# Kernel tuning notes

Hardware: AMD Instinct MI355X
Metric: run time of the kernel (lower is better)

The kernel has to match this reference:

```python
import jax, jax.numpy as jnp
import numpy as np

N = 100000   # num nodes (in_channels)
D = 128      # out_channels
H = 2 * D    # hidden dim
E = 1600000  # num edges


def gcn_conv(x, W, b, src, dst, dinv):
    """PyG GCNConv: linear -> symmetric-normalized aggregation (with self loops) -> +bias."""
    xw = x @ W                                   # [N, out]
    norm = dinv[src] * dinv[dst]                 # [E]
    msg = xw[src] * norm[:, None]                # [E, out]  gather + scale
    agg = jax.ops.segment_sum(msg, dst, num_segments=N)  # scatter-add to targets
    agg = agg + xw * (dinv * dinv)[:, None]      # self-loop contribution
    return agg + b


def setup_inputs() -> dict:
    key = jax.random.key(0)
    k1, k2, k3, k4, k5, k6 = jax.random.split(key, 6)
    emb = jax.random.normal(k1, (N, D), dtype=jnp.float32)
    # Glorot-ish scaled weights
    W1 = jax.random.normal(k2, (D, H), dtype=jnp.float32) * (1.0 / np.sqrt(D))
    b1 = jnp.zeros((H,), dtype=jnp.float32)
    W2 = jax.random.normal(k3, (H, D), dtype=jnp.float32) * (1.0 / np.sqrt(H))
    b2 = jnp.zeros((D,), dtype=jnp.float32)
    edge_index = jax.random.randint(k4, (2, E), 0, N, dtype=jnp.int32).astype(jnp.int64)
    return {"emb": emb, "W1": W1, "b1": b1, "W2": W2, "b2": b2, "edge_index": edge_index}


def reference(emb, W1, b1, W2, b2, edge_index):
    src = edge_index[0]
    dst = edge_index[1]
    # degrees include the self loop added by GCNConv (add_self_loops=True)
    deg = jax.ops.segment_sum(jnp.ones((E,), dtype=emb.dtype), dst, num_segments=N) + 1.0
    dinv = jax.lax.rsqrt(deg)                    # deg >= 1, always finite
    x = gcn_conv(emb, W1, b1, src, dst, dinv)    # [N, 2D]
    x = jax.nn.relu(x)
    out = gcn_conv(x, W2, b2, src, dst, dinv)    # [N, D]
    return out
```

## Files before the change

### kernel.cpp

```cpp
#include <hip/hip_runtime.h>
#include <hip/hip_bf16.h>

#define NN 100000
#define DD 128
#define HH 256

#define NBKT 391
#define ABLK 128

typedef _Float16 half_t;
typedef _Float16 half8 __attribute__((ext_vector_type(8)));
typedef _Float16 half4_t __attribute__((ext_vector_type(4)));
typedef float floatx4 __attribute__((ext_vector_type(4)));


__global__ __launch_bounds__(256) void hist_bkt(const int* __restrict__ dst,
                                                int* __restrict__ cnt,
                                                int* __restrict__ tot,
                                                int E, int epb) {
    __shared__ int h[NBKT];
    for (int i = threadIdx.x; i < NBKT; i += 256) h[i] = 0;
    __syncthreads();
    int base = blockIdx.x * epb;
    int end = min(base + epb, E);
    for (int e = base + (int)threadIdx.x; e < end; e += 256)
        atomicAdd(&h[dst[e] >> 8], 1);
    __syncthreads();
    for (int i = threadIdx.x; i < NBKT; i += 256) {
        int v = h[i];
        cnt[i * ABLK + blockIdx.x] = v;
        if (v) atomicAdd(&tot[i], v);
    }
}

__global__ __launch_bounds__(512) void scan_all(const int* __restrict__ tot,
                                                const int* __restrict__ cnt,
                                                int* __restrict__ bktStart,
                                                int* __restrict__ blockOff) {
    __shared__ int s[512];
    int b = blockIdx.x, t = threadIdx.x;
    int v = (t < NBKT) ? tot[t] : 0;
    s[t] = v;
    __syncthreads();
    for (int off = 1; off < 512; off <<= 1) {
        int u = (t >= off) ? s[t - off] : 0;
        __syncthreads();
        s[t] += u;
        __syncthreads();
    }
    int bs = (b > 0) ? s[b - 1] : 0;
    int tail = s[NBKT - 1];
    __syncthreads();
    if (t == 0) {
        bktStart[b] = bs;
        if (b == NBKT - 1) bktStart[NBKT] = tail;
    }
    int c = (t < ABLK) ? cnt[b * ABLK + t] : 0;
    s[t] = c;
    __syncthreads();
    for (int off = 1; off < 512; off <<= 1) {
        int u = (t >= off) ? s[t - off] : 0;
        __syncthreads();
        s[t] += u;
        __syncthreads();
    }
    if (t < ABLK) blockOff[b * ABLK + t] = bs + s[t] - c;
}

__global__ __launch_bounds__(256) void part_edges(const int* __restrict__ src,
                                                  const int* __restrict__ dst,
                                                  const int* __restrict__ blockOff,
                                                  int* __restrict__ epk4,
                                                  int E, int epb) {
    __shared__ int lbase[NBKT];
    for (int i = threadIdx.x; i < NBKT; i += 256)
        lbase[i] = blockOff[i * ABLK + blockIdx.x];
    __syncthreads();
    int base = blockIdx.x * epb;
    int end = min(base + epb, E);
    for (int e = base + (int)threadIdx.x; e < end; e += 256) {
        int d = dst[e];
        int p = atomicAdd(&lbase[d >> 8], 1);
        epk4[p] = src[e] | ((d & 255) << 17);
    }
}

__global__ __launch_bounds__(256) void build_csr(const int* __restrict__ epk4,
                                                 const int* __restrict__ bktStart,
                                                 int* __restrict__ offsets,
                                                 float* __restrict__ dinv,
                                                 int* __restrict__ eidx, int N) {
    __shared__ int ncnt[256];
    __shared__ int noff[256];
    __shared__ int cur[256];
    int b = blockIdx.x, t = threadIdx.x;
    int n0 = b << 8;
    int estart = bktStart[b], eend = bktStart[b + 1];
    ncnt[t] = 0;
    __syncthreads();
    for (int e = estart + t; e < eend; e += 256)
        atomicAdd(&ncnt[epk4[e] >> 17], 1);
    __syncthreads();
    int c = ncnt[t];
    noff[t] = c;
    __syncthreads();
    for (int off = 1; off < 256; off <<= 1) {
        int u = (t >= off) ? noff[t - off] : 0;
        __syncthreads();
        noff[t] += u;
        __syncthreads();
    }
    int myoff = estart + noff[t] - c;
    cur[t] = myoff;
    int node = n0 + t;
    if (node < N) {
        offsets[node] = myoff;
        dinv[node] = rsqrtf((float)c + 1.0f);
        if (node == N - 1) offsets[N] = eend;
    }
    __syncthreads();
    for (int e = estart + t; e < eend; e += 256) {
        int p = epk4[e];
        int pos = atomicAdd(&cur[p >> 17], 1);
        eidx[pos] = p & 0x1FFFF;
    }
}

__global__ __launch_bounds__(256) void f2h_scale(const float* __restrict__ in,
                                                 const float* __restrict__ dinv,
                                                 half_t* __restrict__ out, int n4) {
    int i = blockIdx.x * 256 + threadIdx.x;
    if (i < n4) {
        float s = dinv[i >> 5];
        float4 v = ((const float4*)in)[i];
        half4_t o = {(half_t)(v.x * s), (half_t)(v.y * s), (half_t)(v.z * s), (half_t)(v.w * s)};
        ((half4_t*)out)[i] = o;
    }
}

__global__ __launch_bounds__(256) void transpose_both(const float* __restrict__ W1,
                                                      const float* __restrict__ W2,
                                                      half_t* __restrict__ W1t,
                                                      half_t* __restrict__ W2t) {
    int i = blockIdx.x * 256 + threadIdx.x;
    if (i < DD * HH) {
        int k = i / HH, c = i - k * HH;
        W1t[(size_t)c * DD + k] = (half_t)W1[i];
    } else if (i < 2 * DD * HH) {
        int j = i - DD * HH;
        int k = j / DD, c = j - k * DD;
        W2t[(size_t)c * HH + k] = (half_t)W2[j];
    }
}

template <int K, int CT, bool BIASRELU>
__global__ __launch_bounds__(256) void gemm_mfma(const half_t* __restrict__ A,
                                                 const half_t* __restrict__ Bt,
                                                 const float* __restrict__ dinv,
                                                 const float* __restrict__ bias,
                                                 half_t* __restrict__ C, int M) {
    constexpr int BK = 64;
    constexpr int LDA = 72;
    __shared__ __align__(16) half_t As[128][LDA];
    __shared__ __align__(16) half_t Bs[64][LDA];

    const int tid = threadIdx.x;
    const int wave = tid >> 6, lane = tid & 63;
    const int wr = wave >> 1, wc = wave & 1;
    const int row0 = blockIdx.y * 128;
    const int col0 = blockIdx.x * 64;
    const int lrow = lane & 15, kq = lane >> 4;

    floatx4 acc[4][2] = {};

    for (int k0 = 0; k0 < K; k0 += BK) {
#pragma unroll
        for (int i = 0; i < 4; ++i) {
            int r = (tid >> 3) + i * 32;
            int kk = (tid & 7) * 8;
            int gr = row0 + r;
            half8 v = {};
            if (gr < M) v = *(const half8*)(A + (size_t)gr * K + k0 + kk);
            *(half8*)&As[r][kk] = v;
        }
#pragma unroll
        for (int i = 0; i < 2; ++i) {
            int n = (tid >> 3) + i * 32;
            int kk = (tid & 7) * 8;
            half8 v = *(const half8*)(Bt + (size_t)(col0 + n) * K + k0 + kk);
            *(half8*)&Bs[n][kk] = v;
        }
        __syncthreads();
#pragma unroll
        for (int ks = 0; ks < 2; ++ks) {
            half8 af[4], bf[2];
#pragma unroll
            for (int i = 0; i < 4; ++i)
                af[i] = *(const half8*)&As[wr * 64 + i * 16 + lrow][ks * 32 + kq * 8];
#pragma unroll
            for (int j = 0; j < 2; ++j)
                bf[j] = *(const half8*)&Bs[wc * 32 + j * 16 + lrow][ks * 32 + kq * 8];
#pragma unroll
            for (int i = 0; i < 4; ++i)
#pragma unroll
                for (int j = 0; j < 2; ++j)
                    acc[i][j] = __builtin_amdgcn_mfma_f32_16x16x32_f16(af[i], bf[j], acc[i][j], 0, 0, 0);
        }
        __syncthreads();
    }

#pragma unroll
    for (int i = 0; i < 4; ++i) {
#pragma unroll
        for (int r = 0; r < 4; ++r) {
            int grow = row0 + wr * 64 + i * 16 + kq * 4 + r;
            if (grow < M) {
                float s = BIASRELU ? 0.f : dinv[grow];
#pragma unroll
                for (int j = 0; j < 2; ++j) {
                    int gcol = col0 + wc * 32 + j * 16 + lrow;
                    float v = acc[i][j][r];
                    if (BIASRELU) v = fmaxf(v + bias[gcol], 0.f);
                    else          v = v * s;
                    C[(size_t)grow * CT + gcol] = (half_t)v;
                }
            }
        }
    }
}

template <bool OUT16>
__global__ __launch_bounds__(256) void gather128(const half_t* __restrict__ y,
                                                 void* __restrict__ outv,
                                                 const int* __restrict__ offsets,
                                                 const int* __restrict__ eidx,
                                                 const float* __restrict__ dinv,
                                                 const float* __restrict__ bias, int N) {
    int node = blockIdx.x * 8 + (threadIdx.x >> 5);
    if (node >= N) return;
    int c = (threadIdx.x & 31) * 4;

    half4_t sv = *(const half4_t*)(y + (size_t)node * DD + c);
    float a0 = (float)sv[0], a1 = (float)sv[1], a2 = (float)sv[2], a3 = (float)sv[3];
    float b0 = 0.f, b1_ = 0.f, b2_ = 0.f, b3 = 0.f;

    int e = offsets[node];
    const int e1 = offsets[node + 1];
    for (; e + 3 < e1; e += 4) {
        int s0 = eidx[e], s1 = eidx[e + 1], s2 = eidx[e + 2], s3 = eidx[e + 3];
        half4_t v0 = *(const half4_t*)(y + (size_t)s0 * DD + c);
        half4_t v1 = *(const half4_t*)(y + (size_t)s1 * DD + c);
        half4_t v2 = *(const half4_t*)(y + (size_t)s2 * DD + c);
        half4_t v3 = *(const half4_t*)(y + (size_t)s3 * DD + c);
        a0 += (float)v0[0]; a1 += (float)v0[1]; a2 += (float)v0[2]; a3 += (float)v0[3];
        b0 += (float)v1[0]; b1_ += (float)v1[1]; b2_ += (float)v1[2]; b3 += (float)v1[3];
        a0 += (float)v2[0]; a1 += (float)v2[1]; a2 += (float)v2[2]; a3 += (float)v2[3];
        b0 += (float)v3[0]; b1_ += (float)v3[1]; b2_ += (float)v3[2]; b3 += (float)v3[3];
    }
    for (; e < e1; ++e) {
        int s0 = eidx[e];
        half4_t v0 = *(const half4_t*)(y + (size_t)s0 * DD + c);
        a0 += (float)v0[0]; a1 += (float)v0[1]; a2 += (float)v0[2]; a3 += (float)v0[3];
    }

    float s = dinv[node];
    float o0 = s * (a0 + b0);
    float o1 = s * (a1 + b1_);
    float o2 = s * (a2 + b2_);
    float o3 = s * (a3 + b3);
    if (OUT16) {
        half4_t o = {(half_t)o0, (half_t)o1, (half_t)o2, (half_t)o3};
        *(half4_t*)((half_t*)outv + (size_t)node * DD + c) = o;
    } else {
        float4 bb = *(const float4*)(bias + c);
        float4 o = make_float4(o0 + bb.x, o1 + bb.y, o2 + bb.z, o3 + bb.w);
        *(float4*)((float*)outv + (size_t)node * DD + c) = o;
    }
}

extern "C" void kernel_launch(void* const* d_in, const int* in_sizes, int n_in,
                              void* d_out, int out_size, void* d_ws, size_t ws_size,
                              hipStream_t stream) {
    const float* emb = (const float*)d_in[0];
    const float* W1  = (const float*)d_in[1];
    const float* b1  = (const float*)d_in[2];
    const float* W2  = (const float*)d_in[3];
    const float* b2  = (const float*)d_in[4];
    const int*   ei  = (const int*)d_in[5];

    const int N = NN;
    const int E = in_sizes[5] / 2;
    const int* src = ei;
    const int* dst = ei + E;

    char* w = (char*)d_ws;
    float*  dinv = (float*)w;  w += 100032 * 4;
    half_t* zh   = (half_t*)w; w += (size_t)NN * DD * 2;
    half_t* g1h  = (half_t*)w; w += (size_t)NN * DD * 2;
    half_t* x1h  = (half_t*)w; w += (size_t)NN * HH * 2;
    half_t* W1t  = (half_t*)w; w += (size_t)DD * HH * 2;
    half_t* W2t  = (half_t*)w; w += (size_t)HH * DD * 2;
    int* offsets = (int*)w;    w += 100032 * 4;
    int* cnt     = (int*)w;    w += (size_t)NBKT * ABLK * 4;
    int* blockOff= (int*)w;    w += (size_t)NBKT * ABLK * 4;
    int* tot     = (int*)w;    w += 512 * 4;
    int* bktStart= (int*)w;    w += 512 * 4;
    int* epk4    = (int*)w;    w += (size_t)E * 4;
    int* eidx    = (int*)w;
    float* out   = (float*)d_out;
    half_t* y2h  = zh;

    const int epb = (E + ABLK - 1) / ABLK;

    hipMemsetAsync(tot, 0, NBKT * sizeof(int), stream);
    hist_bkt<<<ABLK, 256, 0, stream>>>(dst, cnt, tot, E, epb);
    scan_all<<<NBKT, 512, 0, stream>>>(tot, cnt, bktStart, blockOff);
    part_edges<<<ABLK, 256, 0, stream>>>(src, dst, blockOff, epk4, E, epb);
    build_csr<<<NBKT, 256, 0, stream>>>(epk4, bktStart, offsets, dinv, eidx, N);

    f2h_scale<<<(NN * DD / 4 + 255) / 256, 256, 0, stream>>>(emb, dinv, zh, NN * DD / 4);
    transpose_both<<<(2 * DD * HH + 255) / 256, 256, 0, stream>>>(W1, W2, W1t, W2t);

    const int gy = (N + 127) / 128;
    const int aggBlocks = (N + 7) / 8;

    gather128<true><<<aggBlocks, 256, 0, stream>>>(zh, g1h, offsets, eidx, dinv, nullptr, N);
    gemm_mfma<DD, HH, true><<<dim3(HH / 64, gy), 256, 0, stream>>>(g1h, W1t, dinv, b1, x1h, N);

    gemm_mfma<HH, DD, false><<<dim3(DD / 64, gy), 256, 0, stream>>>(x1h, W2t, dinv, nullptr, y2h, N);
    gather128<false><<<aggBlocks, 256, 0, stream>>>(y2h, (void*)out, offsets, eidx, dinv, b2, N);
}
```

Baseline: 393.7 us.

## Swizzle GEMM block order, unroll gather by 8, double partition blocks

Remaps GEMM block indices so groups of eight row tiles sweep all column tiles together, improving L2 reuse of A rows. The grid height is padded to 784 row tiles so the grouping divides evenly, relying on the existing M bounds check for the extra tiles. The gather loop gains an 8-way unrolled section to put more independent loads in flight. The edge histogram and partition kernels now use twice as many blocks. Extra rows do no work but cost launch slots, and the wider unroll raises register use.

```diff
diff --git a/kernel.cpp b/kernel.cpp
--- a/kernel.cpp
+++ b/kernel.cpp
@@ -6,7 +6,7 @@
 #define HH 256
 
 #define NBKT 391
-#define ABLK 128
+#define ABLK 256
 
 typedef _Float16 half_t;
 typedef _Float16 half8 __attribute__((ext_vector_type(8)));
@@ -153,7 +153,7 @@
     }
 }
 
-template <int K, int CT, bool BIASRELU>
+template <int K, int CT, int NCB, bool BIASRELU>
 __global__ __launch_bounds__(256) void gemm_mfma(const half_t* __restrict__ A,
                                                  const half_t* __restrict__ Bt,
                                                  const float* __restrict__ dinv,
@@ -167,8 +167,12 @@
     const int tid = threadIdx.x;
     const int wave = tid >> 6, lane = tid & 63;
     const int wr = wave >> 1, wc = wave & 1;
-    const int row0 = blockIdx.y * 128;
-    const int col0 = blockIdx.x * 64;
+
+    const int d = blockIdx.x + NCB * blockIdx.y;
+    const int rp = (d / (8 * NCB)) * 8 + (d & 7);
+    const int cc = (d >> 3) % NCB;
+    const int row0 = rp * 128;
+    const int col0 = cc * 64;
     const int lrow = lane & 15, kq = lane >> 4;
 
     floatx4 acc[4][2] = {};
@@ -246,6 +250,26 @@
 
     int e = offsets[node];
     const int e1 = offsets[node + 1];
+    for (; e + 7 < e1; e += 8) {
+        int s0 = eidx[e],     s1 = eidx[e + 1], s2 = eidx[e + 2], s3 = eidx[e + 3];
+        int s4 = eidx[e + 4], s5 = eidx[e + 5], s6 = eidx[e + 6], s7 = eidx[e + 7];
+        half4_t v0 = *(const half4_t*)(y + (size_t)s0 * DD + c);
+        half4_t v1 = *(const half4_t*)(y + (size_t)s1 * DD + c);
+        half4_t v2 = *(const half4_t*)(y + (size_t)s2 * DD + c);
+        half4_t v3 = *(const half4_t*)(y + (size_t)s3 * DD + c);
+        half4_t v4 = *(const half4_t*)(y + (size_t)s4 * DD + c);
+        half4_t v5 = *(const half4_t*)(y + (size_t)s5 * DD + c);
+        half4_t v6 = *(const half4_t*)(y + (size_t)s6 * DD + c);
+        half4_t v7 = *(const half4_t*)(y + (size_t)s7 * DD + c);
+        a0 += (float)v0[0]; a1 += (float)v0[1]; a2 += (float)v0[2]; a3 += (float)v0[3];
+        b0 += (float)v1[0]; b1_ += (float)v1[1]; b2_ += (float)v1[2]; b3 += (float)v1[3];
+        a0 += (float)v2[0]; a1 += (float)v2[1]; a2 += (float)v2[2]; a3 += (float)v2[3];
+        b0 += (float)v3[0]; b1_ += (float)v3[1]; b2_ += (float)v3[2]; b3 += (float)v3[3];
+        a0 += (float)v4[0]; a1 += (float)v4[1]; a2 += (float)v4[2]; a3 += (float)v4[3];
+        b0 += (float)v5[0]; b1_ += (float)v5[1]; b2_ += (float)v5[2]; b3 += (float)v5[3];
+        a0 += (float)v6[0]; a1 += (float)v6[1]; a2 += (float)v6[2]; a3 += (float)v6[3];
+        b0 += (float)v7[0]; b1_ += (float)v7[1]; b2_ += (float)v7[2]; b3 += (float)v7[3];
+    }
     for (; e + 3 < e1; e += 4) {
         int s0 = eidx[e], s1 = eidx[e + 1], s2 = eidx[e + 2], s3 = eidx[e + 3];
         half4_t v0 = *(const half4_t*)(y + (size_t)s0 * DD + c);
@@ -321,12 +345,12 @@
     f2h_scale<<<(NN * DD / 4 + 255) / 256, 256, 0, stream>>>(emb, dinv, zh, NN * DD / 4);
     transpose_both<<<(2 * DD * HH + 255) / 256, 256, 0, stream>>>(W1, W2, W1t, W2t);
 
-    const int gy = (N + 127) / 128;
+    const int gyp = 784;
     const int aggBlocks = (N + 7) / 8;
 
     gather128<true><<<aggBlocks, 256, 0, stream>>>(zh, g1h, offsets, eidx, dinv, nullptr, N);
-    gemm_mfma<DD, HH, true><<<dim3(HH / 64, gy), 256, 0, stream>>>(g1h, W1t, dinv, b1, x1h, N);
-
-    gemm_mfma<HH, DD, false><<<dim3(DD / 64, gy), 256, 0, stream>>>(x1h, W2t, dinv, nullptr, y2h, N);
+    gemm_mfma<DD, HH, 4, true><<<dim3(4, gyp), 256, 0, stream>>>(g1h, W1t, dinv, b1, x1h, N);
+
+    gemm_mfma<HH, DD, 2, false><<<dim3(2, gyp), 256, 0, stream>>>(x1h, W2t, dinv, nullptr, y2h, N);
     gather128<false><<<aggBlocks, 256, 0, stream>>>(y2h, (void*)out, offsets, eidx, dinv, b2, N);
 }
```

Measured after the change: 359.8 us. 1.09x faster.
